# Performance work log

Hardware: AMD Instinct MI355X
Metric: run time of the kernel (lower is better)

The kernel has to match this reference:

```python
import jax, jax.numpy as jnp
import numpy as np

STATE_DIM = 64; ACTION_DIM = 16; DET = 512; STOCH = 64; HID = 512
B = 128; T = 512


def _lin(key, out_d, in_d):
    k1, k2 = jax.random.split(key)
    lim = 1.0 / np.sqrt(in_d)
    w = jax.random.uniform(k1, (out_d, in_d), minval=-lim, maxval=lim, dtype=jnp.float32)
    b = jax.random.uniform(k2, (out_d,), minval=-lim, maxval=lim, dtype=jnp.float32)
    return w, b


def setup_inputs() -> dict:
    key = jax.random.key(0)
    ks = jax.random.split(key, 12)
    enc_w, enc_b = _lin(ks[0], HID, STATE_DIM)
    dec_w, dec_b = _lin(ks[1], STATE_DIM + 2, DET + STOCH)
    pri_enc_w, pri_enc_b = _lin(ks[2], DET, STOCH + ACTION_DIM)
    gru_wi, gru_bi = _lin(ks[3], 3 * DET, DET)
    gru_wh, gru_bh = _lin(ks[4], 3 * DET, DET)
    pri_d1_w, pri_d1_b = _lin(ks[5], HID, DET)
    pri_d2_w, pri_d2_b = _lin(ks[6], 2 * STOCH, HID)
    pos_enc_w, pos_enc_b = _lin(ks[7], HID, DET + HID)
    pos_dec_w, pos_dec_b = _lin(ks[8], 2 * STOCH, HID)
    observation = jax.random.normal(ks[9], (B, T, STATE_DIM), dtype=jnp.float32)
    actions = jax.random.normal(ks[10], (B, T, ACTION_DIM), dtype=jnp.float32)
    eps = jax.random.normal(ks[11], (B, T, STOCH), dtype=jnp.float32)
    return dict(observation=observation, actions=actions, eps=eps,
                enc_w=enc_w, enc_b=enc_b, dec_w=dec_w, dec_b=dec_b,
                pri_enc_w=pri_enc_w, pri_enc_b=pri_enc_b,
                gru_wi=gru_wi, gru_bi=gru_bi, gru_wh=gru_wh, gru_bh=gru_bh,
                pri_d1_w=pri_d1_w, pri_d1_b=pri_d1_b,
                pri_d2_w=pri_d2_w, pri_d2_b=pri_d2_b,
                pos_enc_w=pos_enc_w, pos_enc_b=pos_enc_b,
                pos_dec_w=pos_dec_w, pos_dec_b=pos_dec_b)


def reference(observation, actions, eps,
              enc_w, enc_b, dec_w, dec_b,
              pri_enc_w, pri_enc_b, gru_wi, gru_bi, gru_wh, gru_bh,
              pri_d1_w, pri_d1_b, pri_d2_w, pri_d2_b,
              pos_enc_w, pos_enc_b, pos_dec_w, pos_dec_b):
    Bsz = observation.shape[0]
    S = eps.shape[-1]
    D = gru_wh.shape[-1]
    # obs embedding: elu(Linear(obs))
    obs_emb = jax.nn.elu(jnp.einsum('bti,hi->bth', observation, enc_w) + enc_b)
    # time-major for scan
    emb_t = jnp.swapaxes(obs_emb, 0, 1)   # [T,B,H]
    act_t = jnp.swapaxes(actions, 0, 1)   # [T,B,A]
    eps_t = jnp.swapaxes(eps, 0, 1)       # [T,B,S]

    def step(carry, inp):
        stoch, det = carry                       # [B,S], [B,D]
        emb, act, e = inp
        # ---- prior: encode (stoch, action), GRU, decode to shift/scale
        x = jnp.concatenate([stoch, act], -1)
        x = jax.nn.elu(x @ pri_enc_w.T + pri_enc_b)          # [B,D]
        gi = x @ gru_wi.T + gru_bi                           # [B,3D]
        gh = det @ gru_wh.T + gru_bh
        ir, iz, ia = jnp.split(gi, 3, -1)
        hr, hz, ha = jnp.split(gh, 3, -1)
        r = jax.nn.sigmoid(ir + hr)
        z = jax.nn.sigmoid(iz + hz)
        n = jnp.tanh(ia + r * ha)
        det = (1.0 - z) * n + z * det                        # new deterministic state
        px = jax.nn.elu(det @ pri_d1_w.T + pri_d1_b)
        px = px @ pri_d2_w.T + pri_d2_b
        p_shift, p_raw = jnp.split(px, 2, -1)
        p_scale = jax.nn.softplus(p_raw) + 0.1
        # ---- posterior: encode (det, embedding) -> shift/scale
        qx = jnp.concatenate([det, emb], -1)
        qx = jax.nn.elu(qx @ pos_enc_w.T + pos_enc_b)
        qx = qx @ pos_dec_w.T + pos_dec_b
        q_shift, q_raw = jnp.split(qx, 2, -1)
        q_scale = jax.nn.softplus(q_raw) + 0.1
        # reparameterized posterior sample
        stoch = q_shift + q_scale * e
        return (stoch, det), (stoch, det, q_shift, q_scale, p_shift, p_scale)

    init = (jnp.zeros((Bsz, S), observation.dtype), jnp.zeros((Bsz, D), observation.dtype))
    _, ys = jax.lax.scan(step, init, (emb_t, act_t, eps_t))
    stochs, dets, q_sh, q_sc, p_sh, p_sc = [jnp.swapaxes(y, 0, 1) for y in ys]
    feats = jnp.concatenate([stochs, dets], -1)              # State.flatten()
    outs = jnp.einsum('btf,of->bto', feats, dec_w) + dec_b   # [B,T,state_dim+2]
    return stochs, dets, outs, q_sh, q_sc, p_sh, p_sc
```

## Files before the change

kernel.cpp:

```cpp
#include <hip/hip_runtime.h>
#include <math.h>

#define BDIM 128
#define TDIM 512
#define BT (BDIM*TDIM)

__device__ __forceinline__ float eluf(float v){ return v > 0.f ? v : expm1f(v); }
__device__ __forceinline__ float softplusf(float v){ return fmaxf(v,0.f) + log1pf(expf(-fabsf(v))); }
__device__ __forceinline__ float sigmoidf(float v){ return 1.f/(1.f+expf(-v)); }

struct GemmP {
  const float* x1; long ldx1;
  const float* x2; long ldx2;
  int split;
  const float* w; int ldw;
  const float* biask;
  const float* bias;
  float* out;  long ldo;
  float* out2;
  int M, N, K, k0;
};

enum { SRC_CONCAT=0, SRC_ELUSUM=1 };
enum { EPI_ELU=0, EPI_PLAIN=1, EPI_PARTIAL=2, EPI_PSCALE=3 };

template<int SRC, int EPI, int BM>
__global__ __launch_bounds__(256) void gemm_k(GemmP pa, GemmP pb)
{
  const GemmP p = (blockIdx.z==0) ? pa : pb;
  constexpr int TM = BM/16;
  __shared__ float  Xs[BM][16];
  __shared__ float4 Ws4[16][16];
  const int tid = threadIdx.x;
  const int nt = tid & 15;
  const int mt = tid >> 4;
  const int n0 = blockIdx.x * 64;
  const int m0 = blockIdx.y * BM;

  float acc[TM][4];
  #pragma unroll
  for (int i=0;i<TM;i++){ acc[i][0]=0.f; acc[i][1]=0.f; acc[i][2]=0.f; acc[i][3]=0.f; }

  const int ktiles = p.K / 16;
  for (int kt=0; kt<ktiles; ++kt){
    const int kbase = p.k0 + kt*16;
    {
      const int nload4 = BM*16/4;
      if (tid < nload4){
        const int mi = tid >> 2;
        const int kk = (tid & 3) * 4;
        const int kabs = kbase + kk;
        float4 v;
        if (SRC == SRC_CONCAT){
          const float* src; long row; int k2;
          if (kabs < p.split){ src = p.x1; row = (long)(m0+mi)*p.ldx1; k2 = kabs; }
          else               { src = p.x2; row = (long)(m0+mi)*p.ldx2; k2 = kabs - p.split; }
          if (src) v = *(const float4*)(src + row + k2);
          else { v.x=0.f; v.y=0.f; v.z=0.f; v.w=0.f; }
        } else {
          const long row = (long)(m0+mi)*p.ldx1;
          float4 a = *(const float4*)(p.x1 + row + kabs);
          float4 b = *(const float4*)(p.x2 + row + kabs);
          v.x = eluf(a.x + b.x + p.biask[kabs+0]);
          v.y = eluf(a.y + b.y + p.biask[kabs+1]);
          v.z = eluf(a.z + b.z + p.biask[kabs+2]);
          v.w = eluf(a.w + b.w + p.biask[kabs+3]);
        }
        *(float4*)(&Xs[mi][kk]) = v;
      }
    }
    {
      const int kk = tid >> 4;
      const int n4 = (tid & 15) * 4;
      const int n = n0 + n4;
      const long base = (long)(kbase + kk) * p.ldw + n;
      float4 v;
      if (n + 3 < p.N) v = *(const float4*)(p.w + base);
      else {
        v.x = (n+0 < p.N) ? p.w[base+0] : 0.f;
        v.y = (n+1 < p.N) ? p.w[base+1] : 0.f;
        v.z = (n+2 < p.N) ? p.w[base+2] : 0.f;
        v.w = (n+3 < p.N) ? p.w[base+3] : 0.f;
      }
      Ws4[kk][tid & 15] = v;
    }
    __syncthreads();
    #pragma unroll
    for (int kk=0; kk<16; ++kk){
      const float4 w4 = Ws4[kk][nt];
      #pragma unroll
      for (int i=0;i<TM;i++){
        const float xv = Xs[mt*TM+i][kk];
        acc[i][0] = fmaf(xv, w4.x, acc[i][0]);
        acc[i][1] = fmaf(xv, w4.y, acc[i][1]);
        acc[i][2] = fmaf(xv, w4.z, acc[i][2]);
        acc[i][3] = fmaf(xv, w4.w, acc[i][3]);
      }
    }
    __syncthreads();
  }
  #pragma unroll
  for (int i=0;i<TM;i++){
    const int m = m0 + mt*TM + i;
    #pragma unroll
    for (int j=0;j<4;j++){
      const int n = n0 + nt*4 + j;
      if (n >= p.N) continue;
      float v = acc[i][j];
      if (EPI == EPI_PARTIAL){
        p.out[(long)m*p.ldo + n] = v;
      } else if (EPI == EPI_ELU){
        p.out[(long)m*p.ldo + n] = eluf(v + p.bias[n]);
      } else if (EPI == EPI_PLAIN){
        p.out[(long)m*p.ldo + n] = v + p.bias[n];
      } else {
        v += p.bias[n];
        if (n < 64) p.out [(long)m*64 + n]      = v;
        else        p.out2[(long)m*64 + (n-64)] = softplusf(v) + 0.1f;
      }
    }
  }
}

__global__ void transpose_k(const float* __restrict__ src, float* __restrict__ dst, int R, int C){
  __shared__ float tile[32][33];
  const int c0 = blockIdx.x*32, r0 = blockIdx.y*32;
  const int tx = threadIdx.x, ty = threadIdx.y;
  for (int i=ty; i<32; i+=8){
    const int r = r0+i, c = c0+tx;
    tile[i][tx] = (r<R && c<C) ? src[(long)r*C + c] : 0.f;
  }
  __syncthreads();
  for (int i=ty; i<32; i+=8){
    const int r = r0+tx, c = c0+i;
    if (r<R && c<C) dst[(long)c*R + r] = tile[tx][i];
  }
}

__global__ void gate_k(const float* __restrict__ gi, const float* __restrict__ gh,
                       const float* __restrict__ det_prev, float* __restrict__ det_out){
  const int idx = blockIdx.x*blockDim.x + threadIdx.x;
  const int b = idx >> 9, n = idx & 511;
  const long g = (long)b*1536 + n;
  const float ir = gi[g], iz = gi[g+512], ia = gi[g+1024];
  const float hr = gh[g], hz = gh[g+512], ha = gh[g+1024];
  const float dp = det_prev ? det_prev[(long)b*TDIM*512 + n] : 0.f;
  const float r = sigmoidf(ir+hr);
  const float z = sigmoidf(iz+hz);
  const float nn = tanhf(ia + r*ha);
  det_out[(long)b*TDIM*512 + n] = (1.f - z)*nn + z*dp;
}

__global__ void stoch_k(const float* __restrict__ qa, const float* __restrict__ qb,
                        const float* __restrict__ pos_dec_b, const float* __restrict__ eps_t,
                        float* __restrict__ q_sh, float* __restrict__ q_sc, float* __restrict__ st){
  const int idx = blockIdx.x*blockDim.x + threadIdx.x;
  const int b = idx >> 6, s = idx & 63;
  const long q = (long)b*128;
  const float v0 = qa[q+s]    + qb[q+s]    + pos_dec_b[s];
  const float v1 = qa[q+64+s] + qb[q+64+s] + pos_dec_b[64+s];
  const float sc = softplusf(v1) + 0.1f;
  const float e  = eps_t[(long)b*TDIM*64 + s];
  const long o = (long)b*TDIM*64 + s;
  q_sh[o] = v0;
  q_sc[o] = sc;
  st[o]   = v0 + sc*e;
}

extern "C" void kernel_launch(void* const* d_in, const int* in_sizes, int n_in,
                              void* d_out, int out_size, void* d_ws, size_t ws_size,
                              hipStream_t stream)
{
  const float* obs       = (const float*)d_in[0];
  const float* act       = (const float*)d_in[1];
  const float* eps       = (const float*)d_in[2];
  const float* enc_w     = (const float*)d_in[3];
  const float* enc_b     = (const float*)d_in[4];
  const float* dec_w     = (const float*)d_in[5];
  const float* dec_b     = (const float*)d_in[6];
  const float* pri_enc_w = (const float*)d_in[7];
  const float* pri_enc_b = (const float*)d_in[8];
  const float* gru_wi    = (const float*)d_in[9];
  const float* gru_bi    = (const float*)d_in[10];
  const float* gru_wh    = (const float*)d_in[11];
  const float* gru_bh    = (const float*)d_in[12];
  const float* pri_d1_w  = (const float*)d_in[13];
  const float* pri_d1_b  = (const float*)d_in[14];
  const float* pri_d2_w  = (const float*)d_in[15];
  const float* pri_d2_b  = (const float*)d_in[16];
  const float* pos_enc_w = (const float*)d_in[17];
  const float* pos_enc_b = (const float*)d_in[18];
  const float* pos_dec_w = (const float*)d_in[19];
  const float* pos_dec_b = (const float*)d_in[20];

  float* out     = (float*)d_out;
  float* o_stoch = out;
  float* o_det   = o_stoch + (long)BT*64;
  float* o_outs  = o_det   + (long)BT*512;
  float* o_qsh   = o_outs  + (long)BT*66;
  float* o_qsc   = o_qsh   + (long)BT*64;
  float* o_psh   = o_qsc   + (long)BT*64;
  float* o_psc   = o_psh   + (long)BT*64;

  float* w = (float*)d_ws;
  float* enc_wT     = w; w += 64*512;
  float* pri_enc_wT = w; w += 80*512;
  float* gru_wiT    = w; w += 512*1536;
  float* gru_whT    = w; w += 512*1536;
  float* pri_d1T    = w; w += 512*512;
  float* pri_d2T    = w; w += 512*128;
  float* pos_encT   = w; w += 1024*512;
  float* pos_decT   = w; w += 512*128;
  float* dec_wT     = w; w += 576*66;
  float* emb        = w; w += (long)BT*512;
  float* x_ws       = w; w += 128*512;
  float* gi_ws      = w; w += 128*1536;
  float* gh_ws      = w; w += 128*1536;
  float* qx1a       = w; w += 128*512;
  float* qx1b       = w; w += 128*512;
  float* qa         = w; w += 128*128;
  float* qb         = w; w += 128*128;

  {
    struct { const float* s; float* d; int R, C; } tps[9] = {
      {enc_w,     enc_wT,     512, 64  },
      {pri_enc_w, pri_enc_wT, 512, 80  },
      {gru_wi,    gru_wiT,    1536,512 },
      {gru_wh,    gru_whT,    1536,512 },
      {pri_d1_w,  pri_d1T,    512, 512 },
      {pri_d2_w,  pri_d2T,    128, 512 },
      {pos_enc_w, pos_encT,   512, 1024},
      {pos_dec_w, pos_decT,   128, 512 },
      {dec_w,     dec_wT,     66,  576 },
    };
    for (int i=0;i<9;i++){
      dim3 g((tps[i].C+31)/32, (tps[i].R+31)/32), b(32,8);
      hipLaunchKernelGGL(transpose_k, g, b, 0, stream, tps[i].s, tps[i].d, tps[i].R, tps[i].C);
    }
  }

  {
    GemmP p{}; p.x1=obs; p.ldx1=64; p.split=64; p.w=enc_wT; p.ldw=512;
    p.bias=enc_b; p.out=emb; p.ldo=512; p.M=BT; p.N=512; p.K=64; p.k0=0;
    hipLaunchKernelGGL((gemm_k<SRC_CONCAT,EPI_ELU,64>), dim3(8,BT/64,1), dim3(256), 0, stream, p, p);
  }

  for (int t=0; t<TDIM; ++t){
    {
      GemmP p{};
      p.x1 = t ? (o_stoch + (long)(t-1)*64) : nullptr; p.ldx1 = (long)TDIM*64;
      p.x2 = act + (long)t*16;                         p.ldx2 = (long)TDIM*16;
      p.split = 64; p.w = pri_enc_wT; p.ldw = 512; p.bias = pri_enc_b;
      p.out = x_ws; p.ldo = 512; p.M = 128; p.N = 512; p.K = 80; p.k0 = 0;
      hipLaunchKernelGGL((gemm_k<SRC_CONCAT,EPI_ELU,16>), dim3(8,8,1), dim3(256), 0, stream, p, p);
    }
    {
      GemmP p0{}; p0.x1 = x_ws; p0.ldx1 = 512; p0.split = 512;
      p0.w = gru_wiT; p0.ldw = 1536; p0.bias = gru_bi;
      p0.out = gi_ws; p0.ldo = 1536; p0.M = 128; p0.N = 1536; p0.K = 512; p0.k0 = 0;
      GemmP p1 = p0;
      p1.x1 = t ? (o_det + (long)(t-1)*512) : nullptr; p1.ldx1 = (long)TDIM*512;
      p1.w = gru_whT; p1.bias = gru_bh; p1.out = gh_ws;
      hipLaunchKernelGGL((gemm_k<SRC_CONCAT,EPI_PLAIN,16>), dim3(24,8,2), dim3(256), 0, stream, p0, p1);
    }
    hipLaunchKernelGGL(gate_k, dim3(256), dim3(256), 0, stream,
        gi_ws, gh_ws, t ? (o_det + (long)(t-1)*512) : nullptr, o_det + (long)t*512);
    {
      GemmP p0{};
      p0.x1 = o_det + (long)t*512; p0.ldx1 = (long)TDIM*512;
      p0.x2 = emb   + (long)t*512; p0.ldx2 = (long)TDIM*512;
      p0.split = 512; p0.w = pos_encT; p0.ldw = 512;
      p0.out = qx1a; p0.ldo = 512; p0.M = 128; p0.N = 512; p0.K = 512; p0.k0 = 0;
      GemmP p1 = p0; p1.k0 = 512; p1.out = qx1b;
      hipLaunchKernelGGL((gemm_k<SRC_CONCAT,EPI_PARTIAL,16>), dim3(8,8,2), dim3(256), 0, stream, p0, p1);
    }
    {
      GemmP p0{};
      p0.x1 = qx1a; p0.ldx1 = 512; p0.x2 = qx1b; p0.ldx2 = 512; p0.biask = pos_enc_b;
      p0.w = pos_decT; p0.ldw = 128;
      p0.out = qa; p0.ldo = 128; p0.M = 128; p0.N = 128; p0.K = 256; p0.k0 = 0;
      GemmP p1 = p0; p1.k0 = 256; p1.out = qb;
      hipLaunchKernelGGL((gemm_k<SRC_ELUSUM,EPI_PARTIAL,16>), dim3(2,8,2), dim3(256), 0, stream, p0, p1);
    }
    hipLaunchKernelGGL(stoch_k, dim3(32), dim3(256), 0, stream,
        qa, qb, pos_dec_b, eps + (long)t*64,
        o_qsh + (long)t*64, o_qsc + (long)t*64, o_stoch + (long)t*64);
  }

  {
    GemmP p{}; p.x1 = o_det; p.ldx1 = 512; p.split = 512;
    p.w = pri_d1T; p.ldw = 512; p.bias = pri_d1_b;
    p.out = emb ; p.ldo = 512; p.M = BT; p.N = 512; p.K = 512; p.k0 = 0;
    hipLaunchKernelGGL((gemm_k<SRC_CONCAT,EPI_ELU,64>), dim3(8,BT/64,1), dim3(256), 0, stream, p, p);
  }
  {
    GemmP p{}; p.x1 = emb; p.ldx1 = 512; p.split = 512;
    p.w = pri_d2T; p.ldw = 128; p.bias = pri_d2_b;
    p.out = o_psh; p.out2 = o_psc; p.M = BT; p.N = 128; p.K = 512; p.k0 = 0;
    hipLaunchKernelGGL((gemm_k<SRC_CONCAT,EPI_PSCALE,64>), dim3(2,BT/64,1), dim3(256), 0, stream, p, p);
  }
  {
    GemmP p{}; p.x1 = o_stoch; p.ldx1 = 64; p.x2 = o_det; p.ldx2 = 512; p.split = 64;
    p.w = dec_wT; p.ldw = 66; p.bias = dec_b;
    p.out = o_outs; p.ldo = 66; p.M = BT; p.N = 66; p.K = 576; p.k0 = 0;
    hipLaunchKernelGGL((gemm_k<SRC_CONCAT,EPI_PLAIN,64>), dim3(2,BT/64,1), dim3(256), 0, stream, p, p);
  }
}
```

Baseline: 42.74 ms.

## Fuse recurrent scan into one persistent cooperative kernel with grid barriers

Replaces the per-timestep launch sequence (six kernels per step across 512 steps) with a single persistent cooperative kernel of 256 blocks. Each block owns two hidden units and synchronises with the others through a hierarchical atomic grid barrier four times per step. State lives in batch-minor ring buffers, and histories are transposed back to the output layout afterwards. This removes about three thousand launches and the intermediate GEMM buffers, in exchange for barrier latency, uncoalesced weight reads from untransposed row-major weights, and extra transpose passes.

```diff
diff --git a/kernel.cpp b/kernel.cpp
--- a/kernel.cpp
+++ b/kernel.cpp
@@ -14,20 +14,18 @@
   const float* x2; long ldx2;
   int split;
   const float* w; int ldw;
-  const float* biask;
   const float* bias;
   float* out;  long ldo;
   float* out2;
   int M, N, K, k0;
 };
 
-enum { SRC_CONCAT=0, SRC_ELUSUM=1 };
-enum { EPI_ELU=0, EPI_PLAIN=1, EPI_PARTIAL=2, EPI_PSCALE=3 };
+enum { SRC_CONCAT=0 };
+enum { EPI_ELU=0, EPI_PLAIN=1, EPI_PSCALE=3, EPI_ELU_T=4 };
 
 template<int SRC, int EPI, int BM>
-__global__ __launch_bounds__(256) void gemm_k(GemmP pa, GemmP pb)
+__global__ __launch_bounds__(256) void gemm_k(GemmP p)
 {
-  const GemmP p = (blockIdx.z==0) ? pa : pb;
   constexpr int TM = BM/16;
   __shared__ float  Xs[BM][16];
   __shared__ float4 Ws4[16][16];
@@ -51,21 +49,11 @@
         const int kk = (tid & 3) * 4;
         const int kabs = kbase + kk;
         float4 v;
-        if (SRC == SRC_CONCAT){
-          const float* src; long row; int k2;
-          if (kabs < p.split){ src = p.x1; row = (long)(m0+mi)*p.ldx1; k2 = kabs; }
-          else               { src = p.x2; row = (long)(m0+mi)*p.ldx2; k2 = kabs - p.split; }
-          if (src) v = *(const float4*)(src + row + k2);
-          else { v.x=0.f; v.y=0.f; v.z=0.f; v.w=0.f; }
-        } else {
-          const long row = (long)(m0+mi)*p.ldx1;
-          float4 a = *(const float4*)(p.x1 + row + kabs);
-          float4 b = *(const float4*)(p.x2 + row + kabs);
-          v.x = eluf(a.x + b.x + p.biask[kabs+0]);
-          v.y = eluf(a.y + b.y + p.biask[kabs+1]);
-          v.z = eluf(a.z + b.z + p.biask[kabs+2]);
-          v.w = eluf(a.w + b.w + p.biask[kabs+3]);
-        }
+        const float* src; long row; int k2;
+        if (kabs < p.split){ src = p.x1; row = (long)(m0+mi)*p.ldx1; k2 = kabs; }
+        else               { src = p.x2; row = (long)(m0+mi)*p.ldx2; k2 = kabs - p.split; }
+        if (src) v = *(const float4*)(src + row + k2);
+        else { v.x=0.f; v.y=0.f; v.z=0.f; v.w=0.f; }
         *(float4*)(&Xs[mi][kk]) = v;
       }
     }
@@ -107,12 +95,12 @@
       const int n = n0 + nt*4 + j;
       if (n >= p.N) continue;
       float v = acc[i][j];
-      if (EPI == EPI_PARTIAL){
-        p.out[(long)m*p.ldo + n] = v;
-      } else if (EPI == EPI_ELU){
+      if (EPI == EPI_ELU){
         p.out[(long)m*p.ldo + n] = eluf(v + p.bias[n]);
       } else if (EPI == EPI_PLAIN){
         p.out[(long)m*p.ldo + n] = v + p.bias[n];
+      } else if (EPI == EPI_ELU_T){
+        p.out[((long)(m & (TDIM-1))*512 + n)*128 + (m >> 9)] = eluf(v + p.bias[n]);
       } else {
         v += p.bias[n];
         if (n < 64) p.out [(long)m*64 + n]      = v;
@@ -137,34 +125,209 @@
   }
 }
 
-__global__ void gate_k(const float* __restrict__ gi, const float* __restrict__ gh,
-                       const float* __restrict__ det_prev, float* __restrict__ det_out){
-  const int idx = blockIdx.x*blockDim.x + threadIdx.x;
-  const int b = idx >> 9, n = idx & 511;
-  const long g = (long)b*1536 + n;
-  const float ir = gi[g], iz = gi[g+512], ia = gi[g+1024];
-  const float hr = gh[g], hz = gh[g+512], ha = gh[g+1024];
-  const float dp = det_prev ? det_prev[(long)b*TDIM*512 + n] : 0.f;
-  const float r = sigmoidf(ir+hr);
-  const float z = sigmoidf(iz+hz);
-  const float nn = tanhf(ia + r*ha);
-  det_out[(long)b*TDIM*512 + n] = (1.f - z)*nn + z*dp;
+struct ScanArgs {
+  const float* __restrict__ act;
+  const float* __restrict__ pri_enc_w;
+  const float* __restrict__ pri_enc_b;
+  const float* __restrict__ gru_wi;
+  const float* __restrict__ gru_bi;
+  const float* __restrict__ gru_wh;
+  const float* __restrict__ gru_bh;
+  const float* __restrict__ pos_enc_w;
+  const float* __restrict__ pos_enc_b;
+  const float* __restrict__ pos_dec_w;
+  const float* __restrict__ pos_dec_b;
+  const float* __restrict__ emb_T;
+  const float* __restrict__ eps_T;
+  float* __restrict__ det_hist;
+  float* __restrict__ st_hist;
+  float* __restrict__ qsh_hist;
+  float* __restrict__ qsc_hist;
+  float* __restrict__ x_ring;
+  float* __restrict__ qx_ring;
+  float* __restrict__ det_ring;
+  float* __restrict__ st_ring;
+  unsigned* bar;
+};
+
+__device__ __forceinline__ void gbar(unsigned* bar, int blk, unsigned phase){
+  __syncthreads();
+  if (threadIdx.x == 0){
+    unsigned* grp  = bar + (blk & 7)*16;
+    unsigned* root = bar + 8*16;
+    unsigned* rel  = bar + 9*16;
+    unsigned v = __hip_atomic_fetch_add(grp, 1u, __ATOMIC_ACQ_REL, __HIP_MEMORY_SCOPE_AGENT);
+    if (v == phase*32u + 31u){
+      unsigned r = __hip_atomic_fetch_add(root, 1u, __ATOMIC_ACQ_REL, __HIP_MEMORY_SCOPE_AGENT);
+      if (r == phase*8u + 7u){
+        __hip_atomic_store(rel, phase+1u, __ATOMIC_RELEASE, __HIP_MEMORY_SCOPE_AGENT);
+      }
+    }
+    while (__hip_atomic_load(rel, __ATOMIC_RELAXED, __HIP_MEMORY_SCOPE_AGENT) <= phase){
+      __builtin_amdgcn_s_sleep(2);
+    }
+  }
+  __syncthreads();
+  __builtin_amdgcn_fence(__ATOMIC_ACQUIRE, "agent");
 }
 
-__global__ void stoch_k(const float* __restrict__ qa, const float* __restrict__ qb,
-                        const float* __restrict__ pos_dec_b, const float* __restrict__ eps_t,
-                        float* __restrict__ q_sh, float* __restrict__ q_sc, float* __restrict__ st){
-  const int idx = blockIdx.x*blockDim.x + threadIdx.x;
-  const int b = idx >> 6, s = idx & 63;
-  const long q = (long)b*128;
-  const float v0 = qa[q+s]    + qb[q+s]    + pos_dec_b[s];
-  const float v1 = qa[q+64+s] + qb[q+64+s] + pos_dec_b[64+s];
-  const float sc = softplusf(v1) + 0.1f;
-  const float e  = eps_t[(long)b*TDIM*64 + s];
-  const long o = (long)b*TDIM*64 + s;
-  q_sh[o] = v0;
-  q_sc[o] = sc;
-  st[o]   = v0 + sc*e;
+__global__ __launch_bounds__(512, 1) void scan_k(ScanArgs a)
+{
+  __shared__ float4 red4[3*512];
+  const int blk = blockIdx.x;
+  const int tid = threadIdx.x;
+  const int r   = tid & 127;
+  const int q   = tid >> 7;
+  const int n0  = blk * 2;
+  unsigned phase = 0;
+
+  for (int t = 0; t < TDIM; ++t){
+    const float* st_prev  = a.st_ring  + ((t+1)&1)*64*128;
+    const float* det_prev = a.det_ring + ((t+1)&1)*512*128;
+    float*       det_cur  = a.det_ring + (t&1)*512*128;
+
+    if (tid < 256){
+      const int c = tid >> 7;
+      const int rr = tid & 127;
+      const int n = n0 + c;
+      const float* wr = a.pri_enc_w + (long)n*80;
+      float acc = a.pri_enc_b[n];
+      #pragma unroll 8
+      for (int k=0;k<64;k++) acc = fmaf(st_prev[k*128 + rr], wr[k], acc);
+      const float* ar = a.act + ((long)rr*TDIM + t)*16;
+      #pragma unroll
+      for (int j=0;j<16;j++) acc = fmaf(ar[j], wr[64+j], acc);
+      a.x_ring[n*128 + rr] = eluf(acc);
+    }
+    gbar(a.bar, blk, phase++);
+
+    {
+      float acc[12];
+      #pragma unroll
+      for (int j=0;j<12;j++) acc[j]=0.f;
+      const int kb = q*128;
+      for (int k=kb; k<kb+128; k+=4){
+        float xv[4], dv[4];
+        #pragma unroll
+        for (int u=0;u<4;u++){ xv[u] = a.x_ring[(k+u)*128 + r]; dv[u] = det_prev[(k+u)*128 + r]; }
+        #pragma unroll
+        for (int u=0;u<4;u++){
+          const int kk = k+u;
+          #pragma unroll
+          for (int c=0;c<2;c++){
+            acc[c*6+0] = fmaf(xv[u], a.gru_wi[(long)(     n0+c)*512 + kk], acc[c*6+0]);
+            acc[c*6+1] = fmaf(xv[u], a.gru_wi[(long)( 512+n0+c)*512 + kk], acc[c*6+1]);
+            acc[c*6+2] = fmaf(xv[u], a.gru_wi[(long)(1024+n0+c)*512 + kk], acc[c*6+2]);
+            acc[c*6+3] = fmaf(dv[u], a.gru_wh[(long)(     n0+c)*512 + kk], acc[c*6+3]);
+            acc[c*6+4] = fmaf(dv[u], a.gru_wh[(long)( 512+n0+c)*512 + kk], acc[c*6+4]);
+            acc[c*6+5] = fmaf(dv[u], a.gru_wh[(long)(1024+n0+c)*512 + kk], acc[c*6+5]);
+          }
+        }
+      }
+      #pragma unroll
+      for (int jg=0;jg<3;jg++)
+        red4[jg*512 + q*128 + r] = make_float4(acc[jg*4+0],acc[jg*4+1],acc[jg*4+2],acc[jg*4+3]);
+      __syncthreads();
+      if (tid < 128){
+        float s[12];
+        #pragma unroll
+        for (int j=0;j<12;j++) s[j]=0.f;
+        #pragma unroll
+        for (int jg=0;jg<3;jg++){
+          #pragma unroll
+          for (int qq=0;qq<4;qq++){
+            float4 v = red4[jg*512 + qq*128 + tid];
+            s[jg*4+0]+=v.x; s[jg*4+1]+=v.y; s[jg*4+2]+=v.z; s[jg*4+3]+=v.w;
+          }
+        }
+        #pragma unroll
+        for (int c=0;c<2;c++){
+          const int n = n0 + c;
+          const float ir = s[c*6+0] + a.gru_bi[n];
+          const float iz = s[c*6+1] + a.gru_bi[512+n];
+          const float ia = s[c*6+2] + a.gru_bi[1024+n];
+          const float hr = s[c*6+3] + a.gru_bh[n];
+          const float hz = s[c*6+4] + a.gru_bh[512+n];
+          const float ha = s[c*6+5] + a.gru_bh[1024+n];
+          const float rg = sigmoidf(ir+hr);
+          const float z  = sigmoidf(iz+hz);
+          const float nn = tanhf(ia + rg*ha);
+          const float dp = det_prev[n*128 + tid];
+          const float dv = (1.f - z)*nn + z*dp;
+          det_cur[n*128 + tid] = dv;
+          a.det_hist[((long)t*512 + n)*128 + tid] = dv;
+        }
+      }
+    }
+    gbar(a.bar, blk, phase++);
+
+    {
+      float a0=0.f, a1=0.f;
+      if (q < 2){
+        const int kb = q*256;
+        for (int k=kb; k<kb+256; k+=4){
+          #pragma unroll
+          for (int u=0;u<4;u++){
+            const float av = det_cur[(k+u)*128 + r];
+            a0 = fmaf(av, a.pos_enc_w[(long)(n0  )*1024 + k+u], a0);
+            a1 = fmaf(av, a.pos_enc_w[(long)(n0+1)*1024 + k+u], a1);
+          }
+        }
+      } else {
+        const int kb = (q-2)*256;
+        const float* embt = a.emb_T + (long)t*512*128;
+        for (int k=kb; k<kb+256; k+=4){
+          #pragma unroll
+          for (int u=0;u<4;u++){
+            const float av = embt[(k+u)*128 + r];
+            a0 = fmaf(av, a.pos_enc_w[(long)(n0  )*1024 + 512 + k+u], a0);
+            a1 = fmaf(av, a.pos_enc_w[(long)(n0+1)*1024 + 512 + k+u], a1);
+          }
+        }
+      }
+      red4[q*128 + r] = make_float4(a0, a1, 0.f, 0.f);
+      __syncthreads();
+      if (tid < 128){
+        float s0=0.f, s1=0.f;
+        #pragma unroll
+        for (int qq=0;qq<4;qq++){ float4 v = red4[qq*128 + tid]; s0+=v.x; s1+=v.y; }
+        a.qx_ring[(n0  )*128 + tid] = eluf(s0 + a.pos_enc_b[n0  ]);
+        a.qx_ring[(n0+1)*128 + tid] = eluf(s1 + a.pos_enc_b[n0+1]);
+      }
+    }
+    gbar(a.bar, blk, phase++);
+
+    if (blk < 64){
+      float a0=0.f, a1=0.f;
+      const int kb = q*128;
+      for (int k=kb; k<kb+128; k+=4){
+        #pragma unroll
+        for (int u=0;u<4;u++){
+          const float qv = a.qx_ring[(k+u)*128 + r];
+          a0 = fmaf(qv, a.pos_dec_w[(long)blk     *512 + k+u], a0);
+          a1 = fmaf(qv, a.pos_dec_w[(long)(blk+64)*512 + k+u], a1);
+        }
+      }
+      red4[q*128 + r] = make_float4(a0, a1, 0.f, 0.f);
+      __syncthreads();
+      if (tid < 128){
+        float sh=0.f, raw=0.f;
+        #pragma unroll
+        for (int qq=0;qq<4;qq++){ float4 v = red4[qq*128 + tid]; sh+=v.x; raw+=v.y; }
+        sh  += a.pos_dec_b[blk];
+        raw += a.pos_dec_b[blk+64];
+        const float sc = softplusf(raw) + 0.1f;
+        const float e  = a.eps_T[((long)t*64 + blk)*128 + tid];
+        const float st = sh + sc*e;
+        const long ho = ((long)t*64 + blk)*128 + tid;
+        a.st_ring[(t&1)*64*128 + blk*128 + tid] = st;
+        a.st_hist[ho]  = st;
+        a.qsh_hist[ho] = sh;
+        a.qsc_hist[ho] = sc;
+      }
+    }
+    gbar(a.bar, blk, phase++);
+  }
 }
 
 extern "C" void kernel_launch(void* const* d_in, const int* in_sizes, int n_in,
@@ -203,106 +366,87 @@
   float* o_psc   = o_psh   + (long)BT*64;
 
   float* w = (float*)d_ws;
-  float* enc_wT     = w; w += 64*512;
-  float* pri_enc_wT = w; w += 80*512;
-  float* gru_wiT    = w; w += 512*1536;
-  float* gru_whT    = w; w += 512*1536;
-  float* pri_d1T    = w; w += 512*512;
-  float* pri_d2T    = w; w += 512*128;
-  float* pos_encT   = w; w += 1024*512;
-  float* pos_decT   = w; w += 512*128;
-  float* dec_wT     = w; w += 576*66;
-  float* emb        = w; w += (long)BT*512;
-  float* x_ws       = w; w += 128*512;
-  float* gi_ws      = w; w += 128*1536;
-  float* gh_ws      = w; w += 128*1536;
-  float* qx1a       = w; w += 128*512;
-  float* qx1b       = w; w += 128*512;
-  float* qa         = w; w += 128*128;
-  float* qb         = w; w += 128*128;
-
-  {
-    struct { const float* s; float* d; int R, C; } tps[9] = {
-      {enc_w,     enc_wT,     512, 64  },
-      {pri_enc_w, pri_enc_wT, 512, 80  },
-      {gru_wi,    gru_wiT,    1536,512 },
-      {gru_wh,    gru_whT,    1536,512 },
-      {pri_d1_w,  pri_d1T,    512, 512 },
-      {pri_d2_w,  pri_d2T,    128, 512 },
-      {pos_enc_w, pos_encT,   512, 1024},
-      {pos_dec_w, pos_decT,   128, 512 },
-      {dec_w,     dec_wT,     66,  576 },
+  float* emb_T    = w; w += (long)TDIM*512*128;
+  float* det_hist = w; w += (long)TDIM*512*128;
+  float* st_hist  = w; w += (long)TDIM*64*128;
+  float* qsh_hist = w; w += (long)TDIM*64*128;
+  float* qsc_hist = w; w += (long)TDIM*64*128;
+  float* eps_T    = w; w += (long)TDIM*64*128;
+  float* x_ring   = w; w += 512*128;
+  float* qx_ring  = w; w += 512*128;
+  float* det_ring = w; w += 2*512*128;
+  float* st_ring  = w; w += 2*64*128;
+  float* enc_wT   = w; w += 64*512;
+  float* pri_d1T  = w; w += 512*512;
+  float* pri_d2T  = w; w += 512*128;
+  float* dec_wT   = w; w += 576*66;
+  unsigned* bar   = (unsigned*)w; w += 256;
+
+  hipMemsetAsync(bar, 0, 256*sizeof(unsigned), stream);
+  hipMemsetAsync(det_ring, 0, 2*512*128*sizeof(float), stream);
+  hipMemsetAsync(st_ring, 0, 2*64*128*sizeof(float), stream);
+
+  {
+    struct { const float* s; float* d; int R, C; } tps[4] = {
+      {enc_w,    enc_wT,  512, 64  },
+      {pri_d1_w, pri_d1T, 512, 512 },
+      {pri_d2_w, pri_d2T, 128, 512 },
+      {dec_w,    dec_wT,  66,  576 },
     };
-    for (int i=0;i<9;i++){
+    for (int i=0;i<4;i++){
       dim3 g((tps[i].C+31)/32, (tps[i].R+31)/32), b(32,8);
       hipLaunchKernelGGL(transpose_k, g, b, 0, stream, tps[i].s, tps[i].d, tps[i].R, tps[i].C);
     }
   }
-
+  hipLaunchKernelGGL(transpose_k, dim3((TDIM*64+31)/32, (128+31)/32), dim3(32,8), 0, stream,
+                     eps, eps_T, 128, TDIM*64);
   {
     GemmP p{}; p.x1=obs; p.ldx1=64; p.split=64; p.w=enc_wT; p.ldw=512;
-    p.bias=enc_b; p.out=emb; p.ldo=512; p.M=BT; p.N=512; p.K=64; p.k0=0;
-    hipLaunchKernelGGL((gemm_k<SRC_CONCAT,EPI_ELU,64>), dim3(8,BT/64,1), dim3(256), 0, stream, p, p);
-  }
-
-  for (int t=0; t<TDIM; ++t){
-    {
-      GemmP p{};
-      p.x1 = t ? (o_stoch + (long)(t-1)*64) : nullptr; p.ldx1 = (long)TDIM*64;
-      p.x2 = act + (long)t*16;                         p.ldx2 = (long)TDIM*16;
-      p.split = 64; p.w = pri_enc_wT; p.ldw = 512; p.bias = pri_enc_b;
-      p.out = x_ws; p.ldo = 512; p.M = 128; p.N = 512; p.K = 80; p.k0 = 0;
-      hipLaunchKernelGGL((gemm_k<SRC_CONCAT,EPI_ELU,16>), dim3(8,8,1), dim3(256), 0, stream, p, p);
-    }
-    {
-      GemmP p0{}; p0.x1 = x_ws; p0.ldx1 = 512; p0.split = 512;
-      p0.w = gru_wiT; p0.ldw = 1536; p0.bias = gru_bi;
-      p0.out = gi_ws; p0.ldo = 1536; p0.M = 128; p0.N = 1536; p0.K = 512; p0.k0 = 0;
-      GemmP p1 = p0;
-      p1.x1 = t ? (o_det + (long)(t-1)*512) : nullptr; p1.ldx1 = (long)TDIM*512;
-      p1.w = gru_whT; p1.bias = gru_bh; p1.out = gh_ws;
-      hipLaunchKernelGGL((gemm_k<SRC_CONCAT,EPI_PLAIN,16>), dim3(24,8,2), dim3(256), 0, stream, p0, p1);
-    }
-    hipLaunchKernelGGL(gate_k, dim3(256), dim3(256), 0, stream,
-        gi_ws, gh_ws, t ? (o_det + (long)(t-1)*512) : nullptr, o_det + (long)t*512);
-    {
-      GemmP p0{};
-      p0.x1 = o_det + (long)t*512; p0.ldx1 = (long)TDIM*512;
-      p0.x2 = emb   + (long)t*512; p0.ldx2 = (long)TDIM*512;
-      p0.split = 512; p0.w = pos_encT; p0.ldw = 512;
-      p0.out = qx1a; p0.ldo = 512; p0.M = 128; p0.N = 512; p0.K = 512; p0.k0 = 0;
-      GemmP p1 = p0; p1.k0 = 512; p1.out = qx1b;
-      hipLaunchKernelGGL((gemm_k<SRC_CONCAT,EPI_PARTIAL,16>), dim3(8,8,2), dim3(256), 0, stream, p0, p1);
-    }
-    {
-      GemmP p0{};
-      p0.x1 = qx1a; p0.ldx1 = 512; p0.x2 = qx1b; p0.ldx2 = 512; p0.biask = pos_enc_b;
-      p0.w = pos_decT; p0.ldw = 128;
-      p0.out = qa; p0.ldo = 128; p0.M = 128; p0.N = 128; p0.K = 256; p0.k0 = 0;
-      GemmP p1 = p0; p1.k0 = 256; p1.out = qb;
-      hipLaunchKernelGGL((gemm_k<SRC_ELUSUM,EPI_PARTIAL,16>), dim3(2,8,2), dim3(256), 0, stream, p0, p1);
-    }
-    hipLaunchKernelGGL(stoch_k, dim3(32), dim3(256), 0, stream,
-        qa, qb, pos_dec_b, eps + (long)t*64,
-        o_qsh + (long)t*64, o_qsc + (long)t*64, o_stoch + (long)t*64);
-  }
-
+    p.bias=enc_b; p.out=emb_T; p.ldo=512; p.M=BT; p.N=512; p.K=64; p.k0=0;
+    hipLaunchKernelGGL((gemm_k<SRC_CONCAT,EPI_ELU_T,64>), dim3(8,BT/64,1), dim3(256), 0, stream, p);
+  }
+
+  {
+    ScanArgs sa;
+    sa.act = act; sa.pri_enc_w = pri_enc_w; sa.pri_enc_b = pri_enc_b;
+    sa.gru_wi = gru_wi; sa.gru_bi = gru_bi; sa.gru_wh = gru_wh; sa.gru_bh = gru_bh;
+    sa.pos_enc_w = pos_enc_w; sa.pos_enc_b = pos_enc_b;
+    sa.pos_dec_w = pos_dec_w; sa.pos_dec_b = pos_dec_b;
+    sa.emb_T = emb_T; sa.eps_T = eps_T;
+    sa.det_hist = det_hist; sa.st_hist = st_hist;
+    sa.qsh_hist = qsh_hist; sa.qsc_hist = qsc_hist;
+    sa.x_ring = x_ring; sa.qx_ring = qx_ring;
+    sa.det_ring = det_ring; sa.st_ring = st_ring; sa.bar = bar;
+    void* kargs[] = { &sa };
+    hipLaunchCooperativeKernel((const void*)scan_k, dim3(256), dim3(512), kargs, 0, stream);
+  }
+
+  hipLaunchKernelGGL(transpose_k, dim3(4, (TDIM*512+31)/32), dim3(32,8), 0, stream,
+                     det_hist, o_det, TDIM*512, 128);
+  hipLaunchKernelGGL(transpose_k, dim3(4, (TDIM*64+31)/32), dim3(32,8), 0, stream,
+                     st_hist, o_stoch, TDIM*64, 128);
+  hipLaunchKernelGGL(transpose_k, dim3(4, (TDIM*64+31)/32), dim3(32,8), 0, stream,
+                     qsh_hist, o_qsh, TDIM*64, 128);
+  hipLaunchKernelGGL(transpose_k, dim3(4, (TDIM*64+31)/32), dim3(32,8), 0, stream,
+                     qsc_hist, o_qsc, TDIM*64, 128);
+
+  float* px = emb_T;
   {
     GemmP p{}; p.x1 = o_det; p.ldx1 = 512; p.split = 512;
     p.w = pri_d1T; p.ldw = 512; p.bias = pri_d1_b;
-    p.out = emb ; p.ldo = 512; p.M = BT; p.N = 512; p.K = 512; p.k0 = 0;
-    hipLaunchKernelGGL((gemm_k<SRC_CONCAT,EPI_ELU,64>), dim3(8,BT/64,1), dim3(256), 0, stream, p, p);
-  }
-  {
-    GemmP p{}; p.x1 = emb; p.ldx1 = 512; p.split = 512;
+    p.out = px; p.ldo = 512; p.M = BT; p.N = 512; p.K = 512; p.k0 = 0;
+    hipLaunchKernelGGL((gemm_k<SRC_CONCAT,EPI_ELU,64>), dim3(8,BT/64,1), dim3(256), 0, stream, p);
+  }
+  {
+    GemmP p{}; p.x1 = px; p.ldx1 = 512; p.split = 512;
     p.w = pri_d2T; p.ldw = 128; p.bias = pri_d2_b;
     p.out = o_psh; p.out2 = o_psc; p.M = BT; p.N = 128; p.K = 512; p.k0 = 0;
-    hipLaunchKernelGGL((gemm_k<SRC_CONCAT,EPI_PSCALE,64>), dim3(2,BT/64,1), dim3(256), 0, stream, p, p);
+    hipLaunchKernelGGL((gemm_k<SRC_CONCAT,EPI_PSCALE,64>), dim3(2,BT/64,1), dim3(256), 0, stream, p);
   }
   {
     GemmP p{}; p.x1 = o_stoch; p.ldx1 = 64; p.x2 = o_det; p.ldx2 = 512; p.split = 64;
     p.w = dec_wT; p.ldw = 66; p.bias = dec_b;
     p.out = o_outs; p.ldo = 66; p.M = BT; p.N = 66; p.K = 576; p.k0 = 0;
-    hipLaunchKernelGGL((gemm_k<SRC_CONCAT,EPI_PLAIN,64>), dim3(2,BT/64,1), dim3(256), 0, stream, p, p);
+    hipLaunchKernelGGL((gemm_k<SRC_CONCAT,EPI_PLAIN,64>), dim3(2,BT/64,1), dim3(256), 0, stream, p);
   }
 }
```

Result: slower. 72.60 ms (+69.9%).
